# Performance work log

Hardware: AMD Instinct MI355X
Metric: run time of the kernel (lower is better)

## Reference

```python
import jax, jax.numpy as jnp
import numpy as np

N = 102400   # total nodes
F = 400      # node features
E = 1638400  # edges
H = 64       # hidden channels
L = 3        # num_layers (hidden convs); +1 final conv to width 1
K = 300      # sort-pool k
NPER = 400   # nodes per graph (uniform graphs)
B = N // NPER
D = H * L + 1  # total_latent_dim = 193


def setup_inputs() -> dict:
    key = jax.random.key(0)
    ks = jax.random.split(key, 20)
    def lin(k, i, o):
        return jax.random.normal(k, (i, o), jnp.float32) / np.sqrt(i)
    inp = {
        "x": jax.random.normal(ks[0], (N, F), jnp.float32),
        "edge_index": jax.random.randint(ks[1], (2, E), 0, N, jnp.int64),
        "W1": lin(ks[2], F, H), "b1": jnp.zeros((H,), jnp.float32),
        "W2": lin(ks[3], H, H), "b2": jnp.zeros((H,), jnp.float32),
        "W3": lin(ks[4], H, H), "b3": jnp.zeros((H,), jnp.float32),
        "W4": lin(ks[5], H, 1), "b4": jnp.zeros((1,), jnp.float32),
        "cw1": jax.random.normal(ks[6], (16, 1, D), jnp.float32) / np.sqrt(D),
        "cb1": jnp.zeros((16,), jnp.float32),
        "cw2": jax.random.normal(ks[7], (32, 16, 5), jnp.float32) / np.sqrt(16 * 5),
        "cb2": jnp.zeros((32,), jnp.float32),
        "mw1": lin(ks[8], 4672, 32), "mb1": jnp.zeros((32,), jnp.float32),
        "mw2": lin(ks[9], 32, 2), "mb2": jnp.zeros((2,), jnp.float32),
    }
    return inp


def _gcn(x, W, b, src, dst, norm):
    h = x @ W                                   # [N, out]
    msg = h[src] * norm[:, None]                # [E', out]
    out = jax.ops.segment_sum(msg, dst, num_segments=N)
    return out + b


def reference(x, edge_index, W1, b1, W2, b2, W3, b3, W4, b4,
              cw1, cb1, cw2, cb2, mw1, mb1, mw2, mb2):
    # GCN normalization with self-loops (D^-1/2 (A+I) D^-1/2)
    loops = jnp.arange(N, dtype=edge_index.dtype)
    src = jnp.concatenate([edge_index[0], loops])
    dst = jnp.concatenate([edge_index[1], loops])
    deg = jax.ops.segment_sum(jnp.ones_like(src, jnp.float32), dst, num_segments=N)
    dis = jax.lax.rsqrt(jnp.maximum(deg, 1.0))
    norm = dis[src] * dis[dst]

    h1 = jnp.tanh(_gcn(x, W1, b1, src, dst, norm))
    h2 = jnp.tanh(_gcn(h1, W2, b2, src, dst, norm))
    h3 = jnp.tanh(_gcn(h2, W3, b3, src, dst, norm))
    h4 = jnp.tanh(_gcn(h3, W4, b4, src, dst, norm))
    feat = jnp.concatenate([h1, h2, h3, h4], axis=-1)  # [N, D]

    # SortAggregation: per-graph sort by last channel (descending), take top-k
    fg = feat.reshape(B, NPER, D)
    order = jnp.argsort(-fg[:, :, -1], axis=1)[:, :K]  # [B, K]
    pooled = jnp.take_along_axis(fg, order[:, :, None], axis=1)  # [B, K, D]
    z = pooled.reshape(B, 1, K * D)

    dn = ("NCH", "OIH", "NCH")
    z = jax.lax.conv_general_dilated(z, cw1, (D,), "VALID", dimension_numbers=dn)
    z = jax.nn.relu(z + cb1[None, :, None])            # [B, 16, K]
    z = jax.lax.reduce_window(z, -jnp.inf, jax.lax.max, (1, 1, 2), (1, 1, 2), "VALID")
    z = jax.lax.conv_general_dilated(z, cw2, (1,), "VALID", dimension_numbers=dn)
    z = jax.nn.relu(z + cb2[None, :, None])            # [B, 32, 146]
    z = z.reshape(B, -1)                               # [B, 4672]
    z = jax.nn.relu(z @ mw1 + mb1)
    return z @ mw2 + mb2                               # [B, 2]
```

## Files before the change

kernel.cpp:

```cpp
#include <hip/hip_runtime.h>
#include <cstdint>
#include <cstddef>

#define Nn 102400
#define Ff 400
#define Ee 1638400
#define Kk 300
#define Bb 256
#define CAP 64

__global__ void deg_k(const int* __restrict__ ei, int* __restrict__ deg) {
    int e = blockIdx.x * 256 + threadIdx.x;
    if (e < Ee) atomicAdd(&deg[ei[Ee + e]], 1);
}

__global__ void dis_k(const int* __restrict__ deg, double* __restrict__ dis) {
    int v = blockIdx.x * 256 + threadIdx.x;
    if (v < Nn) dis[v] = 1.0 / sqrt((double)(deg[v] + 1));
}

__global__ void scat_k(const int* __restrict__ ei, int* __restrict__ fill,
                       int* __restrict__ csr) {
    int e = blockIdx.x * 256 + threadIdx.x;
    if (e >= Ee) return;
    int s = ei[e], d = ei[Ee + e];
    int p = atomicAdd(&fill[d], 1);
    if (p < CAP) csr[(size_t)d * CAP + p] = s;
}

__global__ __launch_bounds__(256) void sortrow_k(const int* __restrict__ deg,
                                                 int* __restrict__ csr) {
    int lane = threadIdx.x & 63;
    int v = blockIdx.x * 4 + (threadIdx.x >> 6);
    int dv = min(deg[v], CAP);
    int key = (lane < dv) ? csr[(size_t)v * CAP + lane] : 0x7FFFFFFF;
#pragma unroll
    for (int k = 2; k <= 64; k <<= 1) {
#pragma unroll
        for (int j = k >> 1; j; j >>= 1) {
            int other = __shfl_xor(key, j);
            bool up = ((lane & k) == 0);
            bool lower = ((lane & j) == 0);
            key = (lower == up) ? min(key, other) : max(key, other);
        }
    }
    if (lane < dv) csr[(size_t)v * CAP + lane] = key;
}

template <typename AT, int CH>
__global__ __launch_bounds__(128) void gemm_t84(const AT* __restrict__ A,
                                                const float* __restrict__ B,
                                                double* __restrict__ C) {
    constexpr int K = 16 * CH;
    __shared__ __align__(16) double As[16][64];
    __shared__ __align__(16) double Bs[16][65];
    int tid = threadIdx.x;
    int tx = tid & 15;
    int ty = tid >> 4;
    int base = blockIdx.x * 64;
    int sr = tid >> 1, sh = tid & 1;
    int bk = tid >> 3, bn = (tid & 7) * 8;
    double acc[8][4] = {};
    for (int ch = 0; ch < CH; ++ch) {
        int k0 = ch * 16;
        double a8[8];
        const AT* ap = A + (size_t)(base + sr) * K + k0 + sh * 8;
        if constexpr (sizeof(AT) == 4) {
            float4 v0 = *(const float4*)(ap);
            float4 v1 = *(const float4*)(ap + 4);
            a8[0] = v0.x; a8[1] = v0.y; a8[2] = v0.z; a8[3] = v0.w;
            a8[4] = v1.x; a8[5] = v1.y; a8[6] = v1.z; a8[7] = v1.w;
        } else {
            double2 d0 = *(const double2*)(ap);
            double2 d1 = *(const double2*)(ap + 2);
            double2 d2 = *(const double2*)(ap + 4);
            double2 d3 = *(const double2*)(ap + 6);
            a8[0] = d0.x; a8[1] = d0.y; a8[2] = d1.x; a8[3] = d1.y;
            a8[4] = d2.x; a8[5] = d2.y; a8[6] = d3.x; a8[7] = d3.y;
        }
        float4 b0 = *(const float4*)(B + (size_t)(k0 + bk) * 64 + bn);
        float4 b1 = *(const float4*)(B + (size_t)(k0 + bk) * 64 + bn + 4);
        __syncthreads();
#pragma unroll
        for (int q = 0; q < 8; ++q) As[sh * 8 + q][sr] = a8[q];
        Bs[bk][bn + 0] = b0.x; Bs[bk][bn + 1] = b0.y;
        Bs[bk][bn + 2] = b0.z; Bs[bk][bn + 3] = b0.w;
        Bs[bk][bn + 4] = b1.x; Bs[bk][bn + 5] = b1.y;
        Bs[bk][bn + 6] = b1.z; Bs[bk][bn + 7] = b1.w;
        __syncthreads();
#pragma unroll
        for (int kk = 0; kk < 16; ++kk) {
            double2 a01 = *(const double2*)&As[kk][ty * 8];
            double2 a23 = *(const double2*)&As[kk][ty * 8 + 2];
            double2 a45 = *(const double2*)&As[kk][ty * 8 + 4];
            double2 a67 = *(const double2*)&As[kk][ty * 8 + 6];
            double2 b01 = *(const double2*)&Bs[kk][tx * 2];
            double2 b23 = *(const double2*)&Bs[kk][32 + tx * 2];
            double av[8] = {a01.x, a01.y, a23.x, a23.y, a45.x, a45.y, a67.x, a67.y};
            double bv[4] = {b01.x, b01.y, b23.x, b23.y};
#pragma unroll
            for (int r = 0; r < 8; ++r)
#pragma unroll
                for (int c = 0; c < 4; ++c) acc[r][c] += av[r] * bv[c];
        }
    }
#pragma unroll
    for (int r = 0; r < 8; ++r) {
        double* cp = C + (size_t)(base + ty * 8 + r) * 64;
        *(double2*)(cp + tx * 2)      = make_double2(acc[r][0], acc[r][1]);
        *(double2*)(cp + 32 + tx * 2) = make_double2(acc[r][2], acc[r][3]);
    }
}

__global__ __launch_bounds__(256) void agg64_k(const double* __restrict__ t,
                                               const float* __restrict__ bias,
                                               const double* __restrict__ dis,
                                               const int* __restrict__ deg,
                                               const int* __restrict__ csr,
                                               double* __restrict__ out,
                                               const float* __restrict__ W4,
                                               double* __restrict__ t4) {
    int lane = threadIdx.x & 63;
    int wv = __builtin_amdgcn_readfirstlane(threadIdx.x >> 6);
    int v = blockIdx.x * 4 + wv;
    int dv = min(deg[v], CAP);
    double dsv = dis[v];
    const int* row = csr + (size_t)v * CAP;
    double acc = 0.0;
    int j = 0;
    for (; j + 8 <= dv; j += 8) {
        int u[8]; double d[8], tv[8];
#pragma unroll
        for (int q = 0; q < 8; ++q) u[q] = row[j + q];
#pragma unroll
        for (int q = 0; q < 8; ++q) tv[q] = t[(size_t)u[q] * 64 + lane];
#pragma unroll
        for (int q = 0; q < 8; ++q) d[q] = dis[u[q]];
#pragma unroll
        for (int q = 0; q < 8; ++q) acc += d[q] * tv[q];
    }
    for (; j < dv; ++j) {
        int u = row[j];
        acc += dis[u] * t[(size_t)u * 64 + lane];
    }
    acc += dsv * t[(size_t)v * 64 + lane];
    double res = tanh((double)bias[lane] + dsv * acc);
    out[(size_t)v * 64 + lane] = res;
    if (t4 != nullptr) {
        double x = res * (double)W4[lane];
#pragma unroll
        for (int o = 32; o > 0; o >>= 1) x += __shfl_xor(x, o);
        if (lane == 0) t4[v] = x;
    }
}

__global__ void agg1_k(const double* __restrict__ t4, const double* __restrict__ dis,
                       const int* __restrict__ deg, const int* __restrict__ csr,
                       const float* __restrict__ b4, double* __restrict__ h4) {
    int v = blockIdx.x * 256 + threadIdx.x;
    if (v >= Nn) return;
    int dv = min(deg[v], CAP);
    double dsv = dis[v];
    double acc = 0.0;
    const int* row = csr + (size_t)v * CAP;
    for (int j = 0; j < dv; ++j) { int u = row[j]; acc += dis[u] * t4[u]; }
    acc += dsv * t4[v];
    h4[v] = tanh((double)b4[0] + dsv * acc);
}

__global__ __launch_bounds__(512) void sort_k(const double* __restrict__ h4,
                                              int* __restrict__ order) {
    __shared__ unsigned long long kv[512];
    __shared__ int ki[512];
    int tid = threadIdx.x, g = blockIdx.x;
    unsigned long long key = ~0ull;
    if (tid < 400) {
        unsigned long long u = (unsigned long long)__double_as_longlong(h4[g * 400 + tid]);
        u = (u & 0x8000000000000000ull) ? ~u : (u | 0x8000000000000000ull);
        key = ~u;
    }
    kv[tid] = key; ki[tid] = tid;
    __syncthreads();
    for (int size = 2; size <= 512; size <<= 1) {
        for (int stride = size >> 1; stride > 0; stride >>= 1) {
            int p = tid ^ stride;
            if (p > tid) {
                bool asc = ((tid & size) == 0);
                unsigned long long a = kv[tid], b = kv[p];
                int ia = ki[tid], ib = ki[p];
                bool gt = (a > b) || (a == b && ia > ib);
                if (gt == asc) { kv[tid] = b; kv[p] = a; ki[tid] = ib; ki[p] = ia; }
            }
            __syncthreads();
        }
    }
    if (tid < Kk) order[g * Kk + tid] = ki[tid];
}

__global__ __launch_bounds__(128) void conv1_k(const double* __restrict__ h1,
                                               const double* __restrict__ h2,
                                               const double* __restrict__ h3,
                                               const double* __restrict__ h4,
                                               const int* __restrict__ order,
                                               const float* __restrict__ cw1,
                                               const float* __restrict__ cb1,
                                               float* __restrict__ z1) {
    __shared__ double wt[193 * 16];
    int tid = threadIdx.x, b = blockIdx.y;
    for (int i = tid; i < 193 * 16; i += 128) {
        int c = i / 193, d = i % 193;
        wt[d * 16 + c] = (double)cw1[i];
    }
    __syncthreads();
    int kpos = blockIdx.x * 128 + tid;
    if (kpos >= Kk) return;
    int n = b * 400 + order[b * Kk + kpos];
    double acc[16];
#pragma unroll
    for (int c = 0; c < 16; ++c) acc[c] = (double)cb1[c];
    const double* bases[3] = {h1 + (size_t)n * 64, h2 + (size_t)n * 64, h3 + (size_t)n * 64};
    for (int r = 0; r < 3; ++r) {
        const double* p = bases[r];
        for (int d = 0; d < 64; ++d) {
            double xv = p[d];
            const double* wp = &wt[((size_t)r * 64 + d) * 16];
#pragma unroll
            for (int c = 0; c < 16; ++c) acc[c] += xv * wp[c];
        }
    }
    double xl = h4[n];
    {
        const double* wp = &wt[192 * 16];
#pragma unroll
        for (int c = 0; c < 16; ++c) acc[c] += xl * wp[c];
    }
#pragma unroll
    for (int c = 0; c < 16; ++c)
        z1[((size_t)b * 16 + c) * 300 + kpos] = (float)fmax(acc[c], 0.0);
}

__global__ __launch_bounds__(256) void tail_k(const float* __restrict__ z1,
                                              const float* __restrict__ cw2,
                                              const float* __restrict__ cb2,
                                              const float* __restrict__ mw1,
                                              const float* __restrict__ mb1,
                                              const float* __restrict__ mw2,
                                              const float* __restrict__ mb2,
                                              float* __restrict__ out) {
    __shared__ float lz[16 * 150];
    __shared__ float lw[2560];
    __shared__ float lz3[4672];
    __shared__ double red[256];
    __shared__ double s4[32];
    int b = blockIdx.x, tid = threadIdx.x;
    for (int i = tid; i < 2400; i += 256) {
        int bc = i / 150, j = i % 150;
        const float* zp = z1 + ((size_t)b * 16 + bc) * 300 + 2 * j;
        lz[i] = fmaxf(zp[0], zp[1]);
    }
    for (int i = tid; i < 2560; i += 256) lw[i] = cw2[i];
    __syncthreads();
    for (int o = tid; o < 4672; o += 256) {
        int co = o / 146, j = o % 146;
        float acc = cb2[co];
#pragma unroll
        for (int ci = 0; ci < 16; ++ci)
#pragma unroll
            for (int tt = 0; tt < 5; ++tt)
                acc += lz[ci * 150 + j + tt] * lw[co * 80 + ci * 5 + tt];
        lz3[o] = fmaxf(acc, 0.f);
    }
    __syncthreads();
    int o = tid & 31, part = tid >> 5;
    double acc = 0.0;
    for (int i = part * 584; i < (part + 1) * 584; ++i)
        acc += (double)lz3[i] * (double)mw1[(size_t)i * 32 + o];
    red[tid] = acc;
    __syncthreads();
    if (tid < 32) {
        double s = 0.0;
#pragma unroll
        for (int p = 0; p < 8; ++p) s += red[p * 32 + tid];
        s4[tid] = fmax(s + (double)mb1[tid], 0.0);
    }
    __syncthreads();
    if (tid < 2) {
        double s = (double)mb2[tid];
#pragma unroll
        for (int j = 0; j < 32; ++j) s += s4[j] * (double)mw2[j * 2 + tid];
        out[b * 2 + tid] = (float)s;
    }
}

extern "C" void kernel_launch(void* const* d_in, const int* in_sizes, int n_in,
                              void* d_out, int out_size, void* d_ws, size_t ws_size,
                              hipStream_t stream) {
    const float* x   = (const float*)d_in[0];
    const int*   ei  = (const int*)d_in[1];
    const float* W1  = (const float*)d_in[2];  const float* b1  = (const float*)d_in[3];
    const float* W2  = (const float*)d_in[4];  const float* b2  = (const float*)d_in[5];
    const float* W3  = (const float*)d_in[6];  const float* b3  = (const float*)d_in[7];
    const float* W4  = (const float*)d_in[8];  const float* b4  = (const float*)d_in[9];
    const float* cw1 = (const float*)d_in[10]; const float* cb1 = (const float*)d_in[11];
    const float* cw2 = (const float*)d_in[12]; const float* cb2 = (const float*)d_in[13];
    const float* mw1 = (const float*)d_in[14]; const float* mb1 = (const float*)d_in[15];
    const float* mw2 = (const float*)d_in[16]; const float* mb2 = (const float*)d_in[17];
    float* out = (float*)d_out;

    const size_t N64 = (size_t)Nn * 64;
    double* t   = (double*)d_ws;
    double* h1  = t + N64;
    double* h2  = h1 + N64;
    double* h3  = h2 + N64;
    double* t4  = h3 + N64;
    double* h4  = t4 + Nn;
    double* dis = h4 + Nn;
    int*   deg  = (int*)(dis + Nn);
    int*   fill = deg + Nn;
    int*   csr  = fill + Nn;
    int*   order = csr + (size_t)Nn * CAP;
    float* z1 = (float*)t;

    hipMemsetAsync(deg, 0, sizeof(int) * (size_t)Nn * 2, stream);

    deg_k <<<Ee / 256, 256, 0, stream>>>(ei, deg);
    dis_k <<<Nn / 256, 256, 0, stream>>>(deg, dis);
    scat_k<<<Ee / 256, 256, 0, stream>>>(ei, fill, csr);
    sortrow_k<<<Nn / 4, 256, 0, stream>>>(deg, csr);

    gemm_t84<float, 25> <<<Nn / 64, 128, 0, stream>>>(x, W1, t);
    agg64_k<<<Nn / 4, 256, 0, stream>>>(t, b1, dis, deg, csr, h1, nullptr, nullptr);
    gemm_t84<double, 4><<<Nn / 64, 128, 0, stream>>>(h1, W2, t);
    agg64_k<<<Nn / 4, 256, 0, stream>>>(t, b2, dis, deg, csr, h2, nullptr, nullptr);
    gemm_t84<double, 4><<<Nn / 64, 128, 0, stream>>>(h2, W3, t);
    agg64_k<<<Nn / 4, 256, 0, stream>>>(t, b3, dis, deg, csr, h3, W4, t4);

    agg1_k<<<Nn / 256, 256, 0, stream>>>(t4, dis, deg, csr, b4, h4);

    sort_k<<<Bb, 512, 0, stream>>>(h4, order);
    conv1_k<<<dim3(3, Bb), 128, 0, stream>>>(h1, h2, h3, h4, order, cw1, cb1, z1);
    tail_k<<<Bb, 256, 0, stream>>>(z1, cw2, cb2, mw1, mb1, mw2, mb2, out);
}
```

Measured before the change: 1.158 ms.

## Drop separate degree pass, double-buffer GEMM tiles, deepen aggregation unroll

Removes the deg_k and dis_k kernels and reuses the scatter fill counters as degrees, with the rsqrt-style normalisation computed inside sortrow_k. This drops one full pass of atomics over the edge list plus one launch. The GEMM is rewritten with 256 threads, a 4x4 per-thread tile and double-buffered shared memory with register prefetch of the next chunk, keeping the A tile in its native type. The aggregation inner loop is unrolled to 16 neighbours with a 4-wide remainder loop to raise memory-level parallelism, at the cost of more registers.

```diff
diff --git a/kernel.cpp b/kernel.cpp
--- a/kernel.cpp
+++ b/kernel.cpp
@@ -8,16 +8,6 @@
 #define Kk 300
 #define Bb 256
 #define CAP 64
-
-__global__ void deg_k(const int* __restrict__ ei, int* __restrict__ deg) {
-    int e = blockIdx.x * 256 + threadIdx.x;
-    if (e < Ee) atomicAdd(&deg[ei[Ee + e]], 1);
-}
-
-__global__ void dis_k(const int* __restrict__ deg, double* __restrict__ dis) {
-    int v = blockIdx.x * 256 + threadIdx.x;
-    if (v < Nn) dis[v] = 1.0 / sqrt((double)(deg[v] + 1));
-}
 
 __global__ void scat_k(const int* __restrict__ ei, int* __restrict__ fill,
                        int* __restrict__ csr) {
@@ -29,10 +19,13 @@
 }
 
 __global__ __launch_bounds__(256) void sortrow_k(const int* __restrict__ deg,
-                                                 int* __restrict__ csr) {
+                                                 int* __restrict__ csr,
+                                                 double* __restrict__ dis) {
     int lane = threadIdx.x & 63;
     int v = blockIdx.x * 4 + (threadIdx.x >> 6);
-    int dv = min(deg[v], CAP);
+    int dvf = deg[v];
+    int dv = min(dvf, CAP);
+    if (lane == 0) dis[v] = 1.0 / sqrt((double)(dvf + 1));
     int key = (lane < dv) ? csr[(size_t)v * CAP + lane] : 0x7FFFFFFF;
 #pragma unroll
     for (int k = 2; k <= 64; k <<= 1) {
@@ -48,65 +41,85 @@
 }
 
 template <typename AT, int CH>
-__global__ __launch_bounds__(128) void gemm_t84(const AT* __restrict__ A,
-                                                const float* __restrict__ B,
-                                                double* __restrict__ C) {
+__global__ __launch_bounds__(256) void gemm_db(const AT* __restrict__ A,
+                                               const float* __restrict__ B,
+                                               double* __restrict__ C) {
     constexpr int K = 16 * CH;
-    __shared__ __align__(16) double As[16][64];
-    __shared__ __align__(16) double Bs[16][65];
+    constexpr bool F32 = (sizeof(AT) == 4);
+    constexpr int APD = F32 ? 76 : 65;
+    __shared__ __align__(16) AT As[2][16 * APD];
+    __shared__ __align__(16) double Bs[2][16 * 65];
     int tid = threadIdx.x;
     int tx = tid & 15;
     int ty = tid >> 4;
     int base = blockIdx.x * 64;
-    int sr = tid >> 1, sh = tid & 1;
-    int bk = tid >> 3, bn = (tid & 7) * 8;
-    double acc[8][4] = {};
+    int sr = tid >> 2, sh = tid & 3;
+    int bk = tid >> 4, bn = (tid & 15) * 4;
+    double acc[4][4] = {};
+
+    AT ar[4];
+    float4 br;
+    const AT* ap0 = A + (size_t)(base + sr) * K + sh * 4;
+    const float* bp0 = B + (size_t)bk * 64 + bn;
+    *(float4*)&br = *(const float4*)(bp0);
+    if constexpr (F32) {
+        float4 v = *(const float4*)(ap0);
+        ar[0] = v.x; ar[1] = v.y; ar[2] = v.z; ar[3] = v.w;
+    } else {
+        double2 d0 = *(const double2*)(ap0);
+        double2 d1 = *(const double2*)(ap0 + 2);
+        ar[0] = d0.x; ar[1] = d0.y; ar[2] = d1.x; ar[3] = d1.y;
+    }
+
+    int p = 0;
     for (int ch = 0; ch < CH; ++ch) {
-        int k0 = ch * 16;
-        double a8[8];
-        const AT* ap = A + (size_t)(base + sr) * K + k0 + sh * 8;
-        if constexpr (sizeof(AT) == 4) {
-            float4 v0 = *(const float4*)(ap);
-            float4 v1 = *(const float4*)(ap + 4);
-            a8[0] = v0.x; a8[1] = v0.y; a8[2] = v0.z; a8[3] = v0.w;
-            a8[4] = v1.x; a8[5] = v1.y; a8[6] = v1.z; a8[7] = v1.w;
-        } else {
-            double2 d0 = *(const double2*)(ap);
-            double2 d1 = *(const double2*)(ap + 2);
-            double2 d2 = *(const double2*)(ap + 4);
-            double2 d3 = *(const double2*)(ap + 6);
-            a8[0] = d0.x; a8[1] = d0.y; a8[2] = d1.x; a8[3] = d1.y;
-            a8[4] = d2.x; a8[5] = d2.y; a8[6] = d3.x; a8[7] = d3.y;
-        }
-        float4 b0 = *(const float4*)(B + (size_t)(k0 + bk) * 64 + bn);
-        float4 b1 = *(const float4*)(B + (size_t)(k0 + bk) * 64 + bn + 4);
+        AT* asw = &As[p][0];
+        double* bsw = &Bs[p][0];
+#pragma unroll
+        for (int q = 0; q < 4; ++q) asw[(sh * 4 + q) * APD + sr] = ar[q];
+        bsw[bk * 65 + bn + 0] = (double)br.x;
+        bsw[bk * 65 + bn + 1] = (double)br.y;
+        bsw[bk * 65 + bn + 2] = (double)br.z;
+        bsw[bk * 65 + bn + 3] = (double)br.w;
         __syncthreads();
-#pragma unroll
-        for (int q = 0; q < 8; ++q) As[sh * 8 + q][sr] = a8[q];
-        Bs[bk][bn + 0] = b0.x; Bs[bk][bn + 1] = b0.y;
-        Bs[bk][bn + 2] = b0.z; Bs[bk][bn + 3] = b0.w;
-        Bs[bk][bn + 4] = b1.x; Bs[bk][bn + 5] = b1.y;
-        Bs[bk][bn + 6] = b1.z; Bs[bk][bn + 7] = b1.w;
+        if (ch + 1 < CH) {
+            const AT* ap = ap0 + (ch + 1) * 16;
+            const float* bp = bp0 + (size_t)(ch + 1) * 16 * 64;
+            *(float4*)&br = *(const float4*)(bp);
+            if constexpr (F32) {
+                float4 v = *(const float4*)(ap);
+                ar[0] = v.x; ar[1] = v.y; ar[2] = v.z; ar[3] = v.w;
+            } else {
+                double2 d0 = *(const double2*)(ap);
+                double2 d1 = *(const double2*)(ap + 2);
+                ar[0] = d0.x; ar[1] = d0.y; ar[2] = d1.x; ar[3] = d1.y;
+            }
+        }
+#pragma unroll
+        for (int kk = 0; kk < 16; ++kk) {
+            double av[4];
+            if constexpr (F32) {
+                float4 a = *(const float4*)&asw[kk * APD + ty * 4];
+                av[0] = a.x; av[1] = a.y; av[2] = a.z; av[3] = a.w;
+            } else {
+                double2 a01 = *(const double2*)&asw[kk * APD + ty * 4];
+                double2 a23 = *(const double2*)&asw[kk * APD + ty * 4 + 2];
+                av[0] = a01.x; av[1] = a01.y; av[2] = a23.x; av[3] = a23.y;
+            }
+            double2 b01 = *(const double2*)&bsw[kk * 65 + tx * 2];
+            double2 b23 = *(const double2*)&bsw[kk * 65 + 32 + tx * 2];
+            double bv[4] = {b01.x, b01.y, b23.x, b23.y};
+#pragma unroll
+            for (int r = 0; r < 4; ++r)
+#pragma unroll
+                for (int c = 0; c < 4; ++c) acc[r][c] += av[r] * bv[c];
+        }
+        p ^= 1;
         __syncthreads();
-#pragma unroll
-        for (int kk = 0; kk < 16; ++kk) {
-            double2 a01 = *(const double2*)&As[kk][ty * 8];
-            double2 a23 = *(const double2*)&As[kk][ty * 8 + 2];
-            double2 a45 = *(const double2*)&As[kk][ty * 8 + 4];
-            double2 a67 = *(const double2*)&As[kk][ty * 8 + 6];
-            double2 b01 = *(const double2*)&Bs[kk][tx * 2];
-            double2 b23 = *(const double2*)&Bs[kk][32 + tx * 2];
-            double av[8] = {a01.x, a01.y, a23.x, a23.y, a45.x, a45.y, a67.x, a67.y};
-            double bv[4] = {b01.x, b01.y, b23.x, b23.y};
-#pragma unroll
-            for (int r = 0; r < 8; ++r)
-#pragma unroll
-                for (int c = 0; c < 4; ++c) acc[r][c] += av[r] * bv[c];
-        }
-    }
-#pragma unroll
-    for (int r = 0; r < 8; ++r) {
-        double* cp = C + (size_t)(base + ty * 8 + r) * 64;
+    }
+#pragma unroll
+    for (int r = 0; r < 4; ++r) {
+        double* cp = C + (size_t)(base + ty * 4 + r) * 64;
         *(double2*)(cp + tx * 2)      = make_double2(acc[r][0], acc[r][1]);
         *(double2*)(cp + 32 + tx * 2) = make_double2(acc[r][2], acc[r][3]);
     }
@@ -128,16 +141,27 @@
     const int* row = csr + (size_t)v * CAP;
     double acc = 0.0;
     int j = 0;
-    for (; j + 8 <= dv; j += 8) {
-        int u[8]; double d[8], tv[8];
-#pragma unroll
-        for (int q = 0; q < 8; ++q) u[q] = row[j + q];
-#pragma unroll
-        for (int q = 0; q < 8; ++q) tv[q] = t[(size_t)u[q] * 64 + lane];
-#pragma unroll
-        for (int q = 0; q < 8; ++q) d[q] = dis[u[q]];
-#pragma unroll
-        for (int q = 0; q < 8; ++q) acc += d[q] * tv[q];
+    for (; j + 16 <= dv; j += 16) {
+        int u[16]; double d[16], tv[16];
+#pragma unroll
+        for (int q = 0; q < 16; ++q) u[q] = row[j + q];
+#pragma unroll
+        for (int q = 0; q < 16; ++q) tv[q] = t[(size_t)u[q] * 64 + lane];
+#pragma unroll
+        for (int q = 0; q < 16; ++q) d[q] = dis[u[q]];
+#pragma unroll
+        for (int q = 0; q < 16; ++q) acc += d[q] * tv[q];
+    }
+    for (; j + 4 <= dv; j += 4) {
+        int u[4]; double d[4], tv[4];
+#pragma unroll
+        for (int q = 0; q < 4; ++q) u[q] = row[j + q];
+#pragma unroll
+        for (int q = 0; q < 4; ++q) tv[q] = t[(size_t)u[q] * 64 + lane];
+#pragma unroll
+        for (int q = 0; q < 4; ++q) d[q] = dis[u[q]];
+#pragma unroll
+        for (int q = 0; q < 4; ++q) acc += d[q] * tv[q];
     }
     for (; j < dv; ++j) {
         int u = row[j];
@@ -315,27 +339,24 @@
     double* t4  = h3 + N64;
     double* h4  = t4 + Nn;
     double* dis = h4 + Nn;
-    int*   deg  = (int*)(dis + Nn);
-    int*   fill = deg + Nn;
+    int*   fill = (int*)(dis + Nn);
     int*   csr  = fill + Nn;
     int*   order = csr + (size_t)Nn * CAP;
     float* z1 = (float*)t;
 
-    hipMemsetAsync(deg, 0, sizeof(int) * (size_t)Nn * 2, stream);
-
-    deg_k <<<Ee / 256, 256, 0, stream>>>(ei, deg);
-    dis_k <<<Nn / 256, 256, 0, stream>>>(deg, dis);
+    hipMemsetAsync(fill, 0, sizeof(int) * (size_t)Nn, stream);
+
     scat_k<<<Ee / 256, 256, 0, stream>>>(ei, fill, csr);
-    sortrow_k<<<Nn / 4, 256, 0, stream>>>(deg, csr);
-
-    gemm_t84<float, 25> <<<Nn / 64, 128, 0, stream>>>(x, W1, t);
-    agg64_k<<<Nn / 4, 256, 0, stream>>>(t, b1, dis, deg, csr, h1, nullptr, nullptr);
-    gemm_t84<double, 4><<<Nn / 64, 128, 0, stream>>>(h1, W2, t);
-    agg64_k<<<Nn / 4, 256, 0, stream>>>(t, b2, dis, deg, csr, h2, nullptr, nullptr);
-    gemm_t84<double, 4><<<Nn / 64, 128, 0, stream>>>(h2, W3, t);
-    agg64_k<<<Nn / 4, 256, 0, stream>>>(t, b3, dis, deg, csr, h3, W4, t4);
-
-    agg1_k<<<Nn / 256, 256, 0, stream>>>(t4, dis, deg, csr, b4, h4);
+    sortrow_k<<<Nn / 4, 256, 0, stream>>>(fill, csr, dis);
+
+    gemm_db<float, 25> <<<Nn / 64, 256, 0, stream>>>(x, W1, t);
+    agg64_k<<<Nn / 4, 256, 0, stream>>>(t, b1, dis, fill, csr, h1, nullptr, nullptr);
+    gemm_db<double, 4><<<Nn / 64, 256, 0, stream>>>(h1, W2, t);
+    agg64_k<<<Nn / 4, 256, 0, stream>>>(t, b2, dis, fill, csr, h2, nullptr, nullptr);
+    gemm_db<double, 4><<<Nn / 64, 256, 0, stream>>>(h2, W3, t);
+    agg64_k<<<Nn / 4, 256, 0, stream>>>(t, b3, dis, fill, csr, h3, W4, t4);
+
+    agg1_k<<<Nn / 256, 256, 0, stream>>>(t4, dis, fill, csr, b4, h4);
 
     sort_k<<<Bb, 512, 0, stream>>>(h4, order);
     conv1_k<<<dim3(3, Bb), 128, 0, stream>>>(h1, h2, h3, h4, order, cw1, cb1, z1);
```

Result: slower. 1.470 ms (+27.0%).
